# Optimization experiments

Measured on AMD Instinct MI355X. Metric: run time of the kernel, lower is better.

Reference implementation:

```python
import jax, jax.numpy as jnp
import numpy as np

EPS = 1e-5
NUM_HEADS = 8
NUM_GROUPS = 32


def conv1x1(x, w, b):
    # x: [B,C,H,W], w: [O,C], b: [O]
    return jnp.einsum('bchw,oc->bohw', x, w) + b[None, :, None, None]


def group_norm(x, w, b, groups=NUM_GROUPS, eps=EPS):
    B, C, H, W = x.shape
    xg = x.reshape(B, groups, C // groups, H, W)
    mean = xg.mean(axis=(2, 3, 4), keepdims=True)
    var = xg.var(axis=(2, 3, 4), keepdims=True)
    xn = ((xg - mean) * jax.lax.rsqrt(var + eps)).reshape(B, C, H, W)
    return xn * w[None, :, None, None] + b[None, :, None, None]


def setup_inputs() -> dict:
    key = jax.random.key(0)
    ks = jax.random.split(key, 12)
    B, C, H, W = 2, 256, 64, 64
    inner = C  # head_dim * num_heads = 32 * 8
    s = 1.0 / np.sqrt(C)
    return {
        'query_feat': jax.random.normal(ks[0], (B, C, H, W), jnp.float32),
        'key_feat': jax.random.normal(ks[1], (B, C, H, W), jnp.float32),
        'q_w': jax.random.normal(ks[2], (inner, C), jnp.float32) * s,
        'q_b': jnp.zeros((inner,), jnp.float32),
        'k_w': jax.random.normal(ks[3], (inner, C), jnp.float32) * s,
        'k_b': jnp.zeros((inner,), jnp.float32),
        'v_w': jax.random.normal(ks[4], (inner, C), jnp.float32) * s,
        'v_b': jnp.zeros((inner,), jnp.float32),
        'out_w': jax.random.normal(ks[5], (C, inner), jnp.float32) * s,
        'out_b': jnp.zeros((C,), jnp.float32),
        'gn_w': jnp.ones((C,), jnp.float32),
        'gn_b': jnp.zeros((C,), jnp.float32),
    }


def reference(query_feat, key_feat, q_w, q_b, k_w, k_b, v_w, v_b, out_w, out_b, gn_w, gn_b):
    B, C, H, W = query_feat.shape
    N = H * W
    h = NUM_HEADS
    d = C // h
    # 1x1 conv projections, then [B, h, N, d]
    def heads(x):
        return x.reshape(B, h, d, N).transpose(0, 1, 3, 2)
    Q = heads(conv1x1(query_feat, q_w, q_b))
    K = heads(conv1x1(key_feat, k_w, k_b))
    V = heads(conv1x1(key_feat, v_w, v_b))
    scores = jnp.einsum('bhnd,bhmd->bhnm', Q, K) * (d ** -0.5)  # [B,h,N,N]
    attn = jax.nn.softmax(scores, axis=-1)
    out = jnp.einsum('bhnm,bhmd->bhnd', attn, V)  # [B,h,N,d]
    out = out.transpose(0, 1, 3, 2).reshape(B, h * d, H, W)
    proj = conv1x1(out, out_w, out_b)
    return group_norm(query_feat + proj, gn_w, gn_b)
```

## Files before the change

kernel.cpp:

```cpp
#include <hip/hip_runtime.h>
#include <math.h>

#define C_DIM 256
#define N_DIM 4096
#define NHEAD 8

using bf16x8 = __attribute__((ext_vector_type(8))) short;
using f32x16 = __attribute__((ext_vector_type(16))) float;

__device__ __forceinline__ short f32_to_bf16(float a) {
    return (short)((__float_as_uint(a) + 0x8000u) >> 16);
}
__device__ __forceinline__ float bf16_to_f32(unsigned short u) {
    return __uint_as_float(((unsigned)u) << 16);
}
__device__ __forceinline__ unsigned pack_trunc(float a, float b) {
    return __builtin_amdgcn_perm(__float_as_uint(b), __float_as_uint(a), 0x07060302u);
}
__device__ __forceinline__ unsigned pack_rnd(float a, float b) {
    return __builtin_amdgcn_perm(__float_as_uint(b) + 0x8000u,
                                 __float_as_uint(a) + 0x8000u, 0x07060302u);
}

__device__ __forceinline__ int SWZ(int m, int c) {
    return (m >> 5) * 8192 + (c >> 4) * 512 + ((c >> 3) & 1) * 256 + (m & 31) * 8 + (c & 7);
}

__global__ __launch_bounds__(256) void prep(
    const float* __restrict__ query, const float* __restrict__ key,
    const float* __restrict__ qw, const float* __restrict__ kw,
    const float* __restrict__ vw, const float* __restrict__ ow,
    short* __restrict__ Qx, short* __restrict__ Kx, short* __restrict__ Wsw)
{
    const int t = threadIdx.x;
    if (blockIdx.z == 4) {
        const int p = blockIdx.y;
        const float* src = (p == 0) ? qw : (p == 1) ? kw : (p == 2) ? vw : ow;
        const int idx = (blockIdx.x * 256 + t) * 4;
        const int o = idx >> 8, c = idx & 255;
        float4 v = *(const float4*)&src[idx];
        short* dst = Wsw + p * 65536 + SWZ(o, c);
        dst[0] = f32_to_bf16(v.x); dst[1] = f32_to_bf16(v.y);
        dst[2] = f32_to_bf16(v.z); dst[3] = f32_to_bf16(v.w);
        return;
    }
    __shared__ unsigned Ts32[32][33];
    const int z = blockIdx.z;
    const float* in = (z < 2) ? query : key;
    short* out = ((z < 2) ? Qx : Kx) + (size_t)(z & 1) * N_DIM * C_DIM;
    const size_t ibase = (size_t)(z & 1) * C_DIM * N_DIM;
    const int n0 = blockIdx.x * 64, c0 = blockIdx.y * 64;
    const int cp = t >> 3, ng = t & 7;

#pragma unroll
    for (int h2 = 0; h2 < 2; ++h2) {
        const int nb = h2 * 32 + ng * 4;
        float4 a = *(const float4*)&in[ibase + (size_t)(c0 + 2 * cp) * N_DIM + n0 + nb];
        float4 b = *(const float4*)&in[ibase + (size_t)(c0 + 2 * cp + 1) * N_DIM + n0 + nb];
        Ts32[ng * 4 + 0][cp] = pack_rnd(a.x, b.x);
        Ts32[ng * 4 + 1][cp] = pack_rnd(a.y, b.y);
        Ts32[ng * 4 + 2][cp] = pack_rnd(a.z, b.z);
        Ts32[ng * 4 + 3][cp] = pack_rnd(a.w, b.w);
        __syncthreads();
        const int nl = t >> 3, cg = t & 7;
        uint4 val;
        val.x = Ts32[nl][cg * 4 + 0];
        val.y = Ts32[nl][cg * 4 + 1];
        val.z = Ts32[nl][cg * 4 + 2];
        val.w = Ts32[nl][cg * 4 + 3];
        *(uint4*)&out[SWZ(n0 + h2 * 32 + nl, c0 + cg * 8)] = val;
        __syncthreads();
    }
}

__global__ __launch_bounds__(256) void qkv_gemm(
    const short* __restrict__ Wsw, const short* __restrict__ Qx,
    const short* __restrict__ Kx,
    const float* __restrict__ q_b, const float* __restrict__ k_b,
    const float* __restrict__ v_b,
    short* __restrict__ Qt, short* __restrict__ Kt, short* __restrict__ Vt,
    float qscale)
{
    const int t = threadIdx.x, w = t >> 6, lane = t & 63;
    const int q2 = lane >> 5, l31 = lane & 31;
    const int proj = blockIdx.z >> 1, b = blockIdx.z & 1;
    const int n0 = blockIdx.x * 64 + (w >> 1) * 32;
    const int o0 = blockIdx.y * 64 + (w & 1) * 32;
    const short* X = ((proj == 0) ? Qx : Kx) + (size_t)b * N_DIM * C_DIM;
    const short* W = Wsw + proj * 65536;
    const float* bias = (proj == 0) ? q_b : (proj == 1) ? k_b : v_b;
    const int xbase = (n0 >> 5) * 8192 + q2 * 256 + l31 * 8;
    const int wbase = (o0 >> 5) * 8192 + q2 * 256 + l31 * 8;

    f32x16 acc;
#pragma unroll
    for (int r = 0; r < 16; ++r) acc[r] = 0.f;

#pragma unroll 4
    for (int kc = 0; kc < C_DIM; kc += 16) {
        bf16x8 xf = *(const bf16x8*)&X[xbase + (kc >> 4) * 512];
        bf16x8 wf = *(const bf16x8*)&W[wbase + (kc >> 4) * 512];
        if (proj == 2)
            acc = __builtin_amdgcn_mfma_f32_32x32x16_bf16(wf, xf, acc, 0, 0, 0);
        else
            acc = __builtin_amdgcn_mfma_f32_32x32x16_bf16(xf, wf, acc, 0, 0, 0);
    }

    const int head = o0 >> 5;
    if (proj < 2) {
        short* OH = ((proj == 0) ? Qt : Kt) + (size_t)(b * NHEAD + head) * N_DIM * 32;
        const float bi = bias[o0 + l31];
        const float sc = (proj == 0) ? qscale : 1.f;
        const int cbase = (n0 >> 5) * 1024 + (l31 >> 4) * 512 + ((l31 >> 3) & 1) * 256 + (l31 & 7);
#pragma unroll
        for (int r = 0; r < 16; ++r) {
            const int qs = (r & 3) + 8 * (r >> 2) + 4 * q2;
            OH[cbase + qs * 8] = f32_to_bf16((acc[r] + bi) * sc);
        }
    } else {
        short* VH = Vt + (size_t)(b * NHEAD + head) * N_DIM * 32;
        const int kbase = (n0 >> 5) * 1024 + (l31 >> 4) * 512 + ((l31 >> 3) & 1) * 256 + (l31 & 7);
#pragma unroll
        for (int r = 0; r < 16; ++r) {
            const int ds = (r & 3) + 8 * (r >> 2) + 4 * q2;
            VH[kbase + ds * 8] = f32_to_bf16(acc[r] + bias[o0 + ds]);
        }
    }
}

__global__ __launch_bounds__(256) void flash_mfma(
    const short* __restrict__ Qt, const short* __restrict__ Kt,
    const short* __restrict__ Vt, short* __restrict__ Opart,
    float* __restrict__ lpart)
{
    const int n0 = blockIdx.x * 128;
    const int h  = blockIdx.y;
    const int z  = blockIdx.z;
    const int b  = z >> 2, s = z & 3;
    const int CHUNK = N_DIM / 4;
    const int t = threadIdx.x, w = t >> 6, lane = t & 63;
    const int q2 = lane >> 5, l31 = lane & 31;
    const int q  = n0 + w * 32 + l31;
    const int bhp = b * NHEAD + h;
    const size_t hb = (size_t)bhp * N_DIM * 32;

    const int qoff = (q >> 5) * 1024 + q2 * 256 + (q & 31) * 8;
    bf16x8 Qf0 = *(const bf16x8*)&Qt[hb + qoff];
    bf16x8 Qf1 = *(const bf16x8*)&Qt[hb + qoff + 512];

    int off = ((s * CHUNK) >> 5) * 1024 + q2 * 256 + l31 * 8;
    bf16x8 Kc0 = *(const bf16x8*)&Kt[hb + off];
    bf16x8 Kc1 = *(const bf16x8*)&Kt[hb + off + 512];
    bf16x8 Vc0 = *(const bf16x8*)&Vt[hb + off];
    bf16x8 Vc1 = *(const bf16x8*)&Vt[hb + off + 512];
    off += 1024;

    f32x16 Of;
#pragma unroll
    for (int r = 0; r < 16; ++r) Of[r] = 0.f;
    float ls = 0.f;

    for (int it = 0; it < CHUNK / 32; ++it) {
        bf16x8 Kn0 = *(const bf16x8*)&Kt[hb + off];
        bf16x8 Kn1 = *(const bf16x8*)&Kt[hb + off + 512];
        bf16x8 Vn0 = *(const bf16x8*)&Vt[hb + off];
        bf16x8 Vn1 = *(const bf16x8*)&Vt[hb + off + 512];
        off += 1024;

        f32x16 acc;
#pragma unroll
        for (int r = 0; r < 16; ++r) acc[r] = 0.f;
        acc = __builtin_amdgcn_mfma_f32_32x32x16_bf16(Kc0, Qf0, acc, 0, 0, 0);
        acc = __builtin_amdgcn_mfma_f32_32x32x16_bf16(Kc1, Qf1, acc, 0, 0, 0);

        float p[16];
#pragma unroll
        for (int r = 0; r < 16; ++r) { p[r] = __builtin_amdgcn_exp2f(acc[r]); ls += p[r]; }

        unsigned u[8], xu[8];
#pragma unroll
        for (int g = 0; g < 8; ++g) u[g] = pack_trunc(p[2 * g], p[2 * g + 1]);
#pragma unroll
        for (int g = 0; g < 8; ++g) xu[g] = (unsigned)__shfl_xor((int)u[g], 32, 64);

        uint4 f0, f1;
        f0.x = q2 ? xu[2] : u[0];  f0.y = q2 ? xu[3] : u[1];
        f0.z = q2 ? u[2]  : xu[0]; f0.w = q2 ? u[3]  : xu[1];
        f1.x = q2 ? xu[6] : u[4];  f1.y = q2 ? xu[7] : u[5];
        f1.z = q2 ? u[6]  : xu[4]; f1.w = q2 ? u[7]  : xu[5];
        bf16x8 Pf0 = __builtin_bit_cast(bf16x8, f0);
        bf16x8 Pf1 = __builtin_bit_cast(bf16x8, f1);

        Of = __builtin_amdgcn_mfma_f32_32x32x16_bf16(Vc0, Pf0, Of, 0, 0, 0);
        Of = __builtin_amdgcn_mfma_f32_32x32x16_bf16(Vc1, Pf1, Of, 0, 0, 0);

        Kc0 = Kn0; Kc1 = Kn1; Vc0 = Vn0; Vc1 = Vn1;
    }

    ls += __shfl_xor(ls, 32, 64);

    const size_t obase = (size_t)(s * 16 + bhp) * (N_DIM * 32)
                       + (size_t)(q >> 5) * 1024 + l31 * 8 + 4 * q2;
#pragma unroll
    for (int g = 0; g < 4; ++g) {
        uint2 st;
        st.x = pack_rnd(Of[4 * g + 0], Of[4 * g + 1]);
        st.y = pack_rnd(Of[4 * g + 2], Of[4 * g + 3]);
        *(uint2*)&Opart[obase + (g >> 1) * 512 + (g & 1) * 256] = st;
    }
    lpart[(size_t)(s * 16 + bhp) * N_DIM + q] = ls;
}

__global__ __launch_bounds__(256) void out_gemm(
    const short* __restrict__ OWsw, const short* __restrict__ Opart,
    const float* __restrict__ lpart, const float* __restrict__ ob,
    const float* __restrict__ query, short* __restrict__ y16)
{
    const int t = threadIdx.x, w = t >> 6, lane = t & 63;
    const int q2 = lane >> 5, l31 = lane & 31;
    const int n0 = blockIdx.x * 32, b = blockIdx.y, oz = blockIdx.z;
    const int o0 = oz * 128 + w * 32;
    const int n = n0 + l31;

    float linv[8];
#pragma unroll
    for (int h = 0; h < 8; ++h) {
        float s = 0.f;
#pragma unroll
        for (int s4 = 0; s4 < 4; ++s4)
            s += lpart[(size_t)(s4 * 16 + b * 8 + h) * N_DIM + n];
        linv[h] = 1.f / s;
    }

    const int abase = (o0 >> 5) * 8192 + q2 * 256 + l31 * 8;
    const size_t SSTR = (size_t)16 * N_DIM * 32;

    f32x16 acc;
#pragma unroll
    for (int r = 0; r < 16; ++r) acc[r] = 0.f;

#pragma unroll
    for (int kc = 0; kc < 16; ++kc) {
        const int head = kc >> 1;
        const size_t base0 = (size_t)(b * 8 + head) * (N_DIM * 32)
                           + (size_t)(n0 >> 5) * 1024 + (kc & 1) * 512
                           + q2 * 256 + l31 * 8;
        bf16x8 p0 = *(const bf16x8*)&Opart[base0];
        bf16x8 p1 = *(const bf16x8*)&Opart[base0 + SSTR];
        bf16x8 p2 = *(const bf16x8*)&Opart[base0 + 2 * SSTR];
        bf16x8 p3 = *(const bf16x8*)&Opart[base0 + 3 * SSTR];
        const float rl = linv[head];
        float p[8];
#pragma unroll
        for (int j = 0; j < 8; ++j) {
            p[j] = (bf16_to_f32((unsigned short)p0[j]) + bf16_to_f32((unsigned short)p1[j]) +
                    bf16_to_f32((unsigned short)p2[j]) + bf16_to_f32((unsigned short)p3[j])) * rl;
        }
        uint4 pk;
        pk.x = pack_rnd(p[0], p[1]);
        pk.y = pack_rnd(p[2], p[3]);
        pk.z = pack_rnd(p[4], p[5]);
        pk.w = pack_rnd(p[6], p[7]);
        bf16x8 bfv = __builtin_bit_cast(bf16x8, pk);
        bf16x8 af = *(const bf16x8*)&OWsw[abase + kc * 512];
        acc = __builtin_amdgcn_mfma_f32_32x32x16_bf16(af, bfv, acc, 0, 0, 0);
    }

    const size_t base = (size_t)b * C_DIM * N_DIM;
#pragma unroll
    for (int r = 0; r < 16; ++r) {
        const int o = o0 + (r & 3) + 8 * (r >> 2) + 4 * q2;
        const size_t addr = base + (size_t)o * N_DIM + n;
        y16[addr] = f32_to_bf16(acc[r] + ob[o] + query[addr]);
    }
}

__global__ __launch_bounds__(256) void gn_stats(
    const short* __restrict__ y16, float* __restrict__ gstats)
{
    const int g = blockIdx.x, b = blockIdx.y;
    const size_t base = ((size_t)b * C_DIM + (size_t)g * 8) * N_DIM;
    const int t = threadIdx.x;
    float sum = 0.f, sumsq = 0.f;
#pragma unroll
    for (int i = 0; i < 32; ++i) {
        const int idx = t + i * 256;
        ushort4 u = *(const ushort4*)&y16[base + (size_t)idx * 4];
        const float v0 = bf16_to_f32(u.x), v1 = bf16_to_f32(u.y);
        const float v2 = bf16_to_f32(u.z), v3 = bf16_to_f32(u.w);
        sum   += v0 + v1 + v2 + v3;
        sumsq += v0 * v0 + v1 * v1 + v2 * v2 + v3 * v3;
    }
#pragma unroll
    for (int off = 1; off < 64; off <<= 1) {
        sum   += __shfl_xor(sum, off, 64);
        sumsq += __shfl_xor(sumsq, off, 64);
    }
    __shared__ float red[8];
    const int wid = t >> 6;
    if ((t & 63) == 0) { red[wid] = sum; red[4 + wid] = sumsq; }
    __syncthreads();
    if (t == 0) {
        const int grp = b * 32 + g;
        gstats[grp * 2 + 0] = red[0] + red[1] + red[2] + red[3];
        gstats[grp * 2 + 1] = red[4] + red[5] + red[6] + red[7];
    }
}

__global__ __launch_bounds__(256) void gn_apply(
    const short* __restrict__ y16, const float* __restrict__ gstats,
    const float* __restrict__ gw, const float* __restrict__ gb,
    float* __restrict__ out)
{
    const int g = blockIdx.x, b = blockIdx.y, sl = blockIdx.z;
    const float s  = gstats[(b * 32 + g) * 2 + 0];
    const float qq = gstats[(b * 32 + g) * 2 + 1];
    const float mean = s * (1.f / 32768.f);
    const float var  = qq * (1.f / 32768.f) - mean * mean;
    const float rstd = rsqrtf(var + 1e-5f);

    const size_t base = ((size_t)b * C_DIM + (size_t)g * 8) * N_DIM + sl * 1024;
    const int t = threadIdx.x;
#pragma unroll
    for (int i = 0; i < 8; ++i) {
        const int idx = t + i * 256;
        const int row = idx >> 8, col = (idx & 255) * 4;
        const size_t a = base + (size_t)row * N_DIM + col;
        const float wv  = gw[g * 8 + row] * rstd;
        const float bb2 = gb[g * 8 + row];
        ushort4 u = *(const ushort4*)&y16[a];
        float4 v;
        v.x = (bf16_to_f32(u.x) - mean) * wv + bb2;
        v.y = (bf16_to_f32(u.y) - mean) * wv + bb2;
        v.z = (bf16_to_f32(u.z) - mean) * wv + bb2;
        v.w = (bf16_to_f32(u.w) - mean) * wv + bb2;
        *(float4*)&out[a] = v;
    }
}

extern "C" void kernel_launch(void* const* d_in, const int* in_sizes, int n_in,
                              void* d_out, int out_size, void* d_ws, size_t ws_size,
                              hipStream_t stream)
{
    const float* query = (const float*)d_in[0];
    const float* key   = (const float*)d_in[1];
    const float* q_w   = (const float*)d_in[2];
    const float* q_b   = (const float*)d_in[3];
    const float* k_w   = (const float*)d_in[4];
    const float* k_b   = (const float*)d_in[5];
    const float* v_w   = (const float*)d_in[6];
    const float* v_b   = (const float*)d_in[7];
    const float* o_w   = (const float*)d_in[8];
    const float* o_b   = (const float*)d_in[9];
    const float* gn_w  = (const float*)d_in[10];
    const float* gn_b  = (const float*)d_in[11];

    char* wsb = (char*)d_ws;
    short* Wsw   = (short*)wsb;
    float* gstats= (float*)(wsb + (3u << 18));
    short* Qx    = (short*)(wsb + (1u  << 20));
    short* Kx    = (short*)(wsb + (5u  << 20));
    short* Qt    = (short*)(wsb + (9u  << 20));
    short* Kt    = (short*)(wsb + (13u << 20));
    short* Vt    = (short*)(wsb + (17u << 20));
    short* Opart = (short*)(wsb + (21u << 20));
    float* lpart = (float*)(wsb + (37u << 20));
    short* y16   = Qx;

    const float qscale = 0.17677669529663687f * 1.4426950408889634f;

    prep<<<dim3(64, 4, 5), 256, 0, stream>>>(query, key, q_w, k_w, v_w, o_w,
                                             Qx, Kx, Wsw);
    qkv_gemm<<<dim3(64, 4, 6), 256, 0, stream>>>(Wsw, Qx, Kx, q_b, k_b, v_b,
                                                 Qt, Kt, Vt, qscale);
    flash_mfma<<<dim3(32, 8, 8), 256, 0, stream>>>(Qt, Kt, Vt, Opart, lpart);
    out_gemm<<<dim3(128, 2, 2), 256, 0, stream>>>(Wsw + 3 * 65536, Opart, lpart,
                                                  o_b, query, y16);
    gn_stats<<<dim3(32, 2), 256, 0, stream>>>(y16, gstats);
    gn_apply<<<dim3(32, 2, 4), 256, 0, stream>>>(y16, gstats, gn_w, gn_b,
                                                 (float*)d_out);
}
```

Measured before the change: 173.4 us.

## Fuse GroupNorm stats/apply into one kernel and vectorize QKV epilogue stores

Measured after the change: 170.3 us. No clear change (-1.8%).

```diff
diff --git a/kernel.cpp b/kernel.cpp
--- a/kernel.cpp
+++ b/kernel.cpp
@@ -101,29 +101,33 @@
         bf16x8 xf = *(const bf16x8*)&X[xbase + (kc >> 4) * 512];
         bf16x8 wf = *(const bf16x8*)&W[wbase + (kc >> 4) * 512];
         if (proj == 2)
+            acc = __builtin_amdgcn_mfma_f32_32x32x16_bf16(xf, wf, acc, 0, 0, 0);
+        else
             acc = __builtin_amdgcn_mfma_f32_32x32x16_bf16(wf, xf, acc, 0, 0, 0);
-        else
-            acc = __builtin_amdgcn_mfma_f32_32x32x16_bf16(xf, wf, acc, 0, 0, 0);
     }
 
     const int head = o0 >> 5;
+    const size_t fbase = (size_t)(n0 >> 5) * 1024 + l31 * 8 + 4 * q2;
     if (proj < 2) {
         short* OH = ((proj == 0) ? Qt : Kt) + (size_t)(b * NHEAD + head) * N_DIM * 32;
-        const float bi = bias[o0 + l31];
         const float sc = (proj == 0) ? qscale : 1.f;
-        const int cbase = (n0 >> 5) * 1024 + (l31 >> 4) * 512 + ((l31 >> 3) & 1) * 256 + (l31 & 7);
-#pragma unroll
-        for (int r = 0; r < 16; ++r) {
-            const int qs = (r & 3) + 8 * (r >> 2) + 4 * q2;
-            OH[cbase + qs * 8] = f32_to_bf16((acc[r] + bi) * sc);
+#pragma unroll
+        for (int g = 0; g < 4; ++g) {
+            float4 bv = *(const float4*)&bias[o0 + 8 * g + 4 * q2];
+            uint2 st;
+            st.x = pack_rnd((acc[4 * g + 0] + bv.x) * sc, (acc[4 * g + 1] + bv.y) * sc);
+            st.y = pack_rnd((acc[4 * g + 2] + bv.z) * sc, (acc[4 * g + 3] + bv.w) * sc);
+            *(uint2*)&OH[fbase + (g >> 1) * 512 + (g & 1) * 256] = st;
         }
     } else {
         short* VH = Vt + (size_t)(b * NHEAD + head) * N_DIM * 32;
-        const int kbase = (n0 >> 5) * 1024 + (l31 >> 4) * 512 + ((l31 >> 3) & 1) * 256 + (l31 & 7);
-#pragma unroll
-        for (int r = 0; r < 16; ++r) {
-            const int ds = (r & 3) + 8 * (r >> 2) + 4 * q2;
-            VH[kbase + ds * 8] = f32_to_bf16(acc[r] + bias[o0 + ds]);
+        const float bi = bias[o0 + l31];
+#pragma unroll
+        for (int g = 0; g < 4; ++g) {
+            uint2 st;
+            st.x = pack_rnd(acc[4 * g + 0] + bi, acc[4 * g + 1] + bi);
+            st.y = pack_rnd(acc[4 * g + 2] + bi, acc[4 * g + 3] + bi);
+            *(uint2*)&VH[fbase + (g >> 1) * 512 + (g & 1) * 256] = st;
         }
     }
 }
@@ -275,16 +279,18 @@
     }
 }
 
-__global__ __launch_bounds__(256) void gn_stats(
-    const short* __restrict__ y16, float* __restrict__ gstats)
+__global__ __launch_bounds__(1024) void gn_fused(
+    const short* __restrict__ y16, const float* __restrict__ gw,
+    const float* __restrict__ gb, float* __restrict__ out)
 {
     const int g = blockIdx.x, b = blockIdx.y;
     const size_t base = ((size_t)b * C_DIM + (size_t)g * 8) * N_DIM;
     const int t = threadIdx.x;
+
     float sum = 0.f, sumsq = 0.f;
 #pragma unroll
-    for (int i = 0; i < 32; ++i) {
-        const int idx = t + i * 256;
+    for (int i = 0; i < 8; ++i) {
+        const int idx = t + i * 1024;
         ushort4 u = *(const ushort4*)&y16[base + (size_t)idx * 4];
         const float v0 = bf16_to_f32(u.x), v1 = bf16_to_f32(u.y);
         const float v2 = bf16_to_f32(u.z), v3 = bf16_to_f32(u.w);
@@ -296,36 +302,27 @@
         sum   += __shfl_xor(sum, off, 64);
         sumsq += __shfl_xor(sumsq, off, 64);
     }
-    __shared__ float red[8];
+    __shared__ float red[34];
     const int wid = t >> 6;
-    if ((t & 63) == 0) { red[wid] = sum; red[4 + wid] = sumsq; }
+    if ((t & 63) == 0) { red[wid] = sum; red[16 + wid] = sumsq; }
     __syncthreads();
     if (t == 0) {
-        const int grp = b * 32 + g;
-        gstats[grp * 2 + 0] = red[0] + red[1] + red[2] + red[3];
-        gstats[grp * 2 + 1] = red[4] + red[5] + red[6] + red[7];
-    }
-}
-
-__global__ __launch_bounds__(256) void gn_apply(
-    const short* __restrict__ y16, const float* __restrict__ gstats,
-    const float* __restrict__ gw, const float* __restrict__ gb,
-    float* __restrict__ out)
-{
-    const int g = blockIdx.x, b = blockIdx.y, sl = blockIdx.z;
-    const float s  = gstats[(b * 32 + g) * 2 + 0];
-    const float qq = gstats[(b * 32 + g) * 2 + 1];
-    const float mean = s * (1.f / 32768.f);
-    const float var  = qq * (1.f / 32768.f) - mean * mean;
-    const float rstd = rsqrtf(var + 1e-5f);
-
-    const size_t base = ((size_t)b * C_DIM + (size_t)g * 8) * N_DIM + sl * 1024;
-    const int t = threadIdx.x;
+        float s = 0.f, qq = 0.f;
+#pragma unroll
+        for (int i = 0; i < 16; ++i) { s += red[i]; qq += red[16 + i]; }
+        const float mean = s * (1.f / 32768.f);
+        const float var  = qq * (1.f / 32768.f) - mean * mean;
+        red[32] = mean;
+        red[33] = rsqrtf(var + 1e-5f);
+    }
+    __syncthreads();
+    const float mean = red[32], rstd = red[33];
+
 #pragma unroll
     for (int i = 0; i < 8; ++i) {
-        const int idx = t + i * 256;
-        const int row = idx >> 8, col = (idx & 255) * 4;
-        const size_t a = base + (size_t)row * N_DIM + col;
+        const int idx = t + i * 1024;
+        const int row = idx >> 10;
+        const size_t a = base + (size_t)idx * 4;
         const float wv  = gw[g * 8 + row] * rstd;
         const float bb2 = gb[g * 8 + row];
         ushort4 u = *(const ushort4*)&y16[a];
@@ -357,7 +354,6 @@
 
     char* wsb = (char*)d_ws;
     short* Wsw   = (short*)wsb;
-    float* gstats= (float*)(wsb + (3u << 18));
     short* Qx    = (short*)(wsb + (1u  << 20));
     short* Kx    = (short*)(wsb + (5u  << 20));
     short* Qt    = (short*)(wsb + (9u  << 20));
@@ -376,7 +372,5 @@
     flash_mfma<<<dim3(32, 8, 8), 256, 0, stream>>>(Qt, Kt, Vt, Opart, lpart);
     out_gemm<<<dim3(128, 2, 2), 256, 0, stream>>>(Wsw + 3 * 65536, Opart, lpart,
                                                   o_b, query, y16);
-    gn_stats<<<dim3(32, 2), 256, 0, stream>>>(y16, gstats);
-    gn_apply<<<dim3(32, 2, 4), 256, 0, stream>>>(y16, gstats, gn_w, gn_b,
-                                                 (float*)d_out);
-}
+    gn_fused<<<dim3(32, 2), 1024, 0, stream>>>(y16, gn_w, gn_b, (float*)d_out);
+}
```
